# Kernel tuning notes

Hardware: AMD Instinct MI355X
Metric: run time of the kernel (lower is better)

Reference implementation:

```python
import jax, jax.numpy as jnp
import numpy as np

N, IN_F, E, EDGE_F, H, C = 50000, 128, 800000, 32, 4, 32
NEG_SLOPE = 0.2
EPS = 1e-16


def setup_inputs() -> dict:
    key = jax.random.key(0)
    ks = jax.random.split(key, 10)
    s = lambda *sh: 1.0 / np.sqrt(sh[-1])
    return {
        "node_features": jax.random.normal(ks[0], (N, IN_F), jnp.float32),
        "edge_features": jax.random.normal(ks[1], (E, EDGE_F), jnp.float32),
        "edge_index": jax.random.randint(ks[2], (2, E), 0, N, jnp.int32),
        # GATConv params
        "W_gat": jax.random.normal(ks[3], (H * C, IN_F), jnp.float32) * s(IN_F),
        "att_src": jax.random.normal(ks[4], (H, C), jnp.float32) * s(C),
        "att_dst": jax.random.normal(ks[5], (H, C), jnp.float32) * s(C),
        "att_edge": jax.random.normal(ks[6], (H, C), jnp.float32) * s(C),
        "bias": jnp.zeros((H * C,), jnp.float32),
        # edge_linear and skip_connection weights
        "W_edge": jax.random.normal(ks[7], (H * C, EDGE_F), jnp.float32) * s(EDGE_F),
        "W_skip": jax.random.normal(ks[8], (H * C, IN_F), jnp.float32) * s(IN_F),
    }


def reference(node_features, edge_features, edge_index, W_gat, att_src, att_dst,
              att_edge, bias, W_edge, W_skip):
    src, dst = edge_index[0], edge_index[1]
    # edge_linear + view(-1, H, C)
    e_attr = (edge_features @ W_edge.T).reshape(E, H, C)
    # GATConv: per-head linear transform of nodes -> [N, H, C]
    x = (node_features @ W_gat.T).reshape(N, H, C)
    # attention logits: a_src.x_i + a_dst.x_j + a_edge.e  -> [E, H]
    a_src = jnp.einsum('nhc,hc->nh', x, att_src)
    a_dst = jnp.einsum('nhc,hc->nh', x, att_dst)
    a_edge = jnp.einsum('ehc,hc->eh', e_attr, att_edge)
    alpha = jax.nn.leaky_relu(a_src[src] + a_dst[dst] + a_edge, NEG_SLOPE)
    # segment softmax over incoming edges of each destination node
    m = jax.ops.segment_max(alpha, dst, num_segments=N)  # [N, H]
    m = jnp.where(jnp.isfinite(m), m, 0.0)
    ex = jnp.exp(alpha - m[dst])
    denom = jax.ops.segment_sum(ex, dst, num_segments=N)  # [N, H]
    attn = ex / (denom[dst] + EPS)  # [E, H]
    # message = alpha * x_src ; scatter-add to destination
    msg = x[src] * attn[:, :, None]  # [E, H, C]
    out = jax.ops.segment_sum(msg, dst, num_segments=N)  # [N, H, C]
    out = out.reshape(N, H * C) + bias  # concat=True
    # skip connection + ELU activation
    out = out + node_features @ W_skip.T
    return jax.nn.elu(out)
```

## Files before the change

### kernel.cpp

```cpp
#include <hip/hip_runtime.h>
#include <hip/hip_bf16.h>

constexpr int N_NODES = 50000;
constexpr int IN_F    = 128;
constexpr long E_EDGES = 800000;
constexpr int EDGE_F  = 32;
constexpr int H_HEADS = 4;
constexpr int C_CH    = 32;
constexpr int HC      = 128;
constexpr float NEG_SLOPE = 0.2f;
constexpr float EPS = 1e-16f;
constexpr int B_HIST = 64;
constexpr int NT_GEMM = (N_NODES + 63) / 64;
constexpr int NB_GEMM2 = (NT_GEMM + 1) / 2;
constexpr int CHUNK  = (int)(E_EDGES / B_HIST);
constexpr int HW4    = N_NODES / 8;
constexpr int NB_SCAN = (N_NODES + 255) / 256;
constexpr int NB_A    = (N_NODES + 3) / 4;
constexpr int NB_EL4  = (int)((E_EDGES + 1023) / 1024);
constexpr int NB_AE5  = (int)((E_EDGES + 511) / 512);
constexpr float SM_SHIFT = 12.0f;

typedef __attribute__((ext_vector_type(8))) short bf16x8;
typedef __attribute__((ext_vector_type(4))) float f32x4;

__device__ __forceinline__ unsigned short f2b(float f) {
    __hip_bfloat16 h = __float2bfloat16(f);
    return *reinterpret_cast<unsigned short*>(&h);
}
__device__ __forceinline__ float b2f_lo(unsigned v) { return __uint_as_float(v << 16); }
__device__ __forceinline__ float b2f_hi(unsigned v) { return __uint_as_float(v & 0xffff0000u); }

__device__ __forceinline__ bf16x8 cvt8(const float* p) {
    float4 a = *(const float4*)p;
    float4 b = *(const float4*)(p + 4);
    bf16x8 f;
    f[0] = (short)f2b(a.x); f[1] = (short)f2b(a.y);
    f[2] = (short)f2b(a.z); f[3] = (short)f2b(a.w);
    f[4] = (short)f2b(b.x); f[5] = (short)f2b(b.y);
    f[6] = (short)f2b(b.z); f[7] = (short)f2b(b.w);
    return f;
}

__global__ __launch_bounds__(512, 4) void mega_kernel(
    const int* __restrict__ dst, unsigned int* __restrict__ histB,
    unsigned short* __restrict__ rank16, const float* __restrict__ ef,
    const float* __restrict__ We, const float* __restrict__ att_edge,
    const float* __restrict__ Wg, const float* __restrict__ Ws,
    float* __restrict__ ae, const float* __restrict__ nf,
    const float* __restrict__ bias, unsigned short* __restrict__ xb,
    float* __restrict__ out)
{
    __shared__ unsigned int h[HW4];
    __shared__ float wf_lds[128];
    const int b = blockIdx.x, t = threadIdx.x;

    if (b < B_HIST) {
        for (int i = t; i < HW4; i += 512) h[i] = 0;
        __syncthreads();
        const int e0 = b * CHUNK;
        for (int i = t * 4; i + 3 < CHUNK; i += 2048) {
            int4 d4 = *(const int4*)(dst + e0 + i);
            ushort4 r4;
            int sh0 = (d4.x & 7) * 4;
            int sh1 = (d4.y & 7) * 4;
            int sh2 = (d4.z & 7) * 4;
            int sh3 = (d4.w & 7) * 4;
            unsigned o0 = atomicAdd(&h[d4.x >> 3], 1u << sh0);
            unsigned o1 = atomicAdd(&h[d4.y >> 3], 1u << sh1);
            unsigned o2 = atomicAdd(&h[d4.z >> 3], 1u << sh2);
            unsigned o3 = atomicAdd(&h[d4.w >> 3], 1u << sh3);
            r4.x = (unsigned short)((o0 >> sh0) & 0xFu);
            r4.y = (unsigned short)((o1 >> sh1) & 0xFu);
            r4.z = (unsigned short)((o2 >> sh2) & 0xFu);
            r4.w = (unsigned short)((o3 >> sh3) & 0xFu);
            *(ushort4*)(rank16 + e0 + i) = r4;
        }
        __syncthreads();
        unsigned int* outp = histB + (size_t)b * HW4;
        for (int i = t; i < HW4; i += 512) outp[i] = h[i];
        return;
    }

    if (b < B_HIST + NB_GEMM2) {
        const int w8 = t >> 6;
        const int l  = t & 63;
        const int lr = l & 15;
        const int lk = l >> 4;
        const int tile = (b - B_HIST) * 2 + (w8 >> 2);
        if (tile >= NT_GEMM) return;
        const int wc = w8 & 3;
        const int n0 = tile * 64;

        f32x4 acc[4][4];
#pragma unroll
        for (int mf = 0; mf < 4; ++mf)
#pragma unroll
            for (int nfr = 0; nfr < 4; ++nfr)
                acc[mf][nfr] = (f32x4){0.f, 0.f, 0.f, 0.f};

#pragma unroll
        for (int ks = 0; ks < 4; ++ks) {
            bf16x8 bfr[4];
#pragma unroll
            for (int nfr = 0; nfr < 4; ++nfr) {
                int gr = wc * 64 + nfr * 16 + lr;
                const float* wp = (gr < HC ? Wg + (size_t)gr * IN_F
                                           : Ws + (size_t)(gr - HC) * IN_F)
                                  + ks * 32 + lk * 8;
                bfr[nfr] = cvt8(wp);
            }
            bf16x8 afr[4];
#pragma unroll
            for (int mf = 0; mf < 4; ++mf) {
                int row = n0 + mf * 16 + lr;
                row = row < N_NODES ? row : N_NODES - 1;
                afr[mf] = cvt8(nf + (size_t)row * IN_F + ks * 32 + lk * 8);
            }
#pragma unroll
            for (int mf = 0; mf < 4; ++mf)
#pragma unroll
                for (int nfr = 0; nfr < 4; ++nfr)
                    acc[mf][nfr] = __builtin_amdgcn_mfma_f32_16x16x32_bf16(
                        afr[mf], bfr[nfr], acc[mf][nfr], 0, 0, 0);
        }

#pragma unroll
        for (int nfr = 0; nfr < 4; ++nfr) {
            const int gc = wc * 64 + nfr * 16 + lr;
            if (gc < HC) {
#pragma unroll
                for (int mf = 0; mf < 4; ++mf)
#pragma unroll
                    for (int r = 0; r < 4; ++r) {
                        int m = n0 + mf * 16 + lk * 4 + r;
                        if (m < N_NODES) xb[(size_t)m * HC + gc] = f2b(acc[mf][nfr][r]);
                    }
            } else {
                const float bv = bias[gc - HC];
#pragma unroll
                for (int mf = 0; mf < 4; ++mf)
#pragma unroll
                    for (int r = 0; r < 4; ++r) {
                        int m = n0 + mf * 16 + lk * 4 + r;
                        if (m < N_NODES) out[(size_t)m * HC + gc - HC] = acc[mf][nfr][r] + bv;
                    }
            }
        }
        return;
    }

    {
        int o = t >> 2, hh = o >> 5, f = o & 31;
        int c0 = (t & 3) * 8;
        float a4 = 0.f;
#pragma unroll
        for (int j = 0; j < 8; ++j) {
            int c = c0 + j;
            a4 = fmaf(We[(hh * C_CH + c) * EDGE_F + f], att_edge[hh * C_CH + c], a4);
        }
        a4 += __shfl_xor(a4, 1);
        a4 += __shfl_xor(a4, 2);
        if ((t & 3) == 0) wf_lds[o] = a4;
    }
    __syncthreads();

    const int l = t & 63, wv = t >> 6;
    const int sub = l & 3, eIdx = l >> 2;
    const long eb = (long)(b - B_HIST - NB_GEMM2) * 512 + wv * 64 + eIdx;
    const float4* ef4 = (const float4*)ef;
    float4 wa[4], wb[4];
#pragma unroll
    for (int hh = 0; hh < 4; ++hh) {
        wa[hh] = *(const float4*)&wf_lds[hh * 32 + sub * 4];
        wb[hh] = *(const float4*)&wf_lds[hh * 32 + 16 + sub * 4];
    }

#pragma unroll
    for (int g = 0; g < 4; ++g) {
        long e = eb + g * 16;
        if (e >= E_EDGES) continue;
        float4 a0 = ef4[e * 8 + sub];
        float4 b0 = ef4[e * 8 + 4 + sub];
        float p[4];
#pragma unroll
        for (int hh = 0; hh < 4; ++hh) {
            float acc = 0.f;
            acc = fmaf(a0.x, wa[hh].x, acc); acc = fmaf(a0.y, wa[hh].y, acc);
            acc = fmaf(a0.z, wa[hh].z, acc); acc = fmaf(a0.w, wa[hh].w, acc);
            acc = fmaf(b0.x, wb[hh].x, acc); acc = fmaf(b0.y, wb[hh].y, acc);
            acc = fmaf(b0.z, wb[hh].z, acc); acc = fmaf(b0.w, wb[hh].w, acc);
            p[hh] = acc;
        }
#pragma unroll
        for (int hh = 0; hh < 4; ++hh) {
            p[hh] += __shfl_xor(p[hh], 1);
            p[hh] += __shfl_xor(p[hh], 2);
        }
        float v0 = (sub == 0) ? p[0] : (sub == 1) ? p[1] : (sub == 2) ? p[2] : p[3];
        ae[e * 4 + sub] = v0;
    }
}

__global__ __launch_bounds__(256) void scan1_a_kernel(
    const unsigned int* __restrict__ histB, int* __restrict__ row_ptr,
    int* __restrict__ blocksum, const unsigned int* __restrict__ xb32,
    const float* __restrict__ att_src, const float* __restrict__ att_dst,
    float* __restrict__ asrc, float* __restrict__ adst)
{
    const int b = blockIdx.x, t = threadIdx.x;
    if (b < NB_SCAN) {
        __shared__ int s[256];
        int i = b * 256 + t;
        int v = 0;
        if (i < N_NODES) {
            int w = i >> 3, sh = (i & 7) * 4;
#pragma unroll 8
            for (int bb = 0; bb < B_HIST; ++bb)
                v += (int)((histB[(size_t)bb * HW4 + w] >> sh) & 0xFu);
        }
        s[t] = v;
        __syncthreads();
#pragma unroll
        for (int off = 1; off < 256; off <<= 1) {
            int u = (t >= off) ? s[t - off] : 0;
            __syncthreads();
            s[t] += u;
            __syncthreads();
        }
        if (i < N_NODES) row_ptr[i] = s[t] - v;
        if (t == 255) blocksum[b] = s[255];
        return;
    }

    const int wave = t >> 6, lane = t & 63;
    const int n = (b - NB_SCAN) * 4 + wave;
    if (n >= N_NODES) return;
    unsigned v = xb32[(size_t)n * 64 + lane];
    float x0 = b2f_lo(v), x1 = b2f_hi(v);
    float2 as = ((const float2*)att_src)[lane];
    float2 ad = ((const float2*)att_dst)[lane];
    float ps = x0 * as.x + x1 * as.y;
    float pd = x0 * ad.x + x1 * ad.y;
#pragma unroll
    for (int off = 1; off < 16; off <<= 1) {
        ps += __shfl_xor(ps, off);
        pd += __shfl_xor(pd, off);
    }
    if ((lane & 15) == 0) {
        asrc[(size_t)n * H_HEADS + (lane >> 4)] = ps;
        adst[(size_t)n * H_HEADS + (lane >> 4)] = pd;
    }
}

__global__ __launch_bounds__(256) void scanF_kernel(int* __restrict__ row_ptr,
                                                    const int* __restrict__ blocksum,
                                                    const unsigned int* __restrict__ histB,
                                                    int* __restrict__ off)
{
    __shared__ int s[256];
    int t = threadIdx.x;
    int v = (t < NB_SCAN) ? blocksum[t] : 0;
    s[t] = v;
    __syncthreads();
#pragma unroll
    for (int o = 1; o < 256; o <<= 1) {
        int u = (t >= o) ? s[t - o] : 0;
        __syncthreads();
        s[t] += u;
        __syncthreads();
    }
    int excl = s[t] - v;
    __syncthreads();
    s[t] = excl;
    __syncthreads();
    const int blockoff = s[blockIdx.x];

    int i = blockIdx.x * 256 + t;
    if (i < N_NODES) {
        int run = row_ptr[i] + blockoff;
        row_ptr[i] = run;
        int w = i >> 3, sh = (i & 7) * 4;
#pragma unroll 8
        for (int b = 0; b < B_HIST; ++b) {
            off[(size_t)b * N_NODES + i] = run;
            run += (int)((histB[(size_t)b * HW4 + w] >> sh) & 0xFu);
        }
    }
    if (i == 0) row_ptr[N_NODES] = (int)E_EDGES;
}

__global__ __launch_bounds__(256) void edge_logits_kernel(
    const int* __restrict__ src, const int* __restrict__ dst,
    const float* __restrict__ ae, const float* __restrict__ asrc,
    const float* __restrict__ adst, const int* __restrict__ off,
    const unsigned short* __restrict__ rank16, uint4* __restrict__ rec4)
{
    const long base = (long)blockIdx.x * 1024 + threadIdx.x;

    int s[4], d[4], rk[4];
    float4 a_e[4];
    bool val[4];
    long ec[4];
#pragma unroll
    for (int j = 0; j < 4; ++j) {
        long e = base + j * 256;
        val[j] = e < E_EDGES;
        ec[j] = val[j] ? e : 0;
        s[j]  = src[ec[j]];
        d[j]  = dst[ec[j]];
        rk[j] = (int)rank16[ec[j]];
        a_e[j] = ((const float4*)ae)[ec[j]];
    }
    float4 as4[4], ad4[4];
    int pos[4];
#pragma unroll
    for (int j = 0; j < 4; ++j) {
        as4[j] = ((const float4*)asrc)[s[j]];
        ad4[j] = ((const float4*)adst)[d[j]];
        int be = (int)(ec[j] / CHUNK);
        pos[j] = off[(size_t)be * N_NODES + d[j]] + rk[j];
    }
#pragma unroll
    for (int j = 0; j < 4; ++j) {
        if (!val[j]) continue;
        float lg[4] = {as4[j].x + ad4[j].x + a_e[j].x, as4[j].y + ad4[j].y + a_e[j].y,
                       as4[j].z + ad4[j].z + a_e[j].z, as4[j].w + ad4[j].w + a_e[j].w};
        uint4 r;
        unsigned* rw = (unsigned*)&r;
#pragma unroll
        for (int h = 0; h < 4; ++h) {
            float al = lg[h] > 0.f ? lg[h] : NEG_SLOPE * lg[h];
            rw[h] = (__float_as_uint(al) & 0xFFFFFF00u)
                  | ((unsigned)(s[j] >> (8 * h)) & 0xFFu);
        }
        rec4[pos[j]] = r;
    }
}

__device__ __forceinline__ void accum8(float* acc, uint4 v, float e) {
    acc[0] = fmaf(b2f_lo(v.x), e, acc[0]);
    acc[1] = fmaf(b2f_hi(v.x), e, acc[1]);
    acc[2] = fmaf(b2f_lo(v.y), e, acc[2]);
    acc[3] = fmaf(b2f_hi(v.y), e, acc[3]);
    acc[4] = fmaf(b2f_lo(v.z), e, acc[4]);
    acc[5] = fmaf(b2f_hi(v.z), e, acc[5]);
    acc[6] = fmaf(b2f_lo(v.w), e, acc[6]);
    acc[7] = fmaf(b2f_hi(v.w), e, acc[7]);
}

__device__ __forceinline__ int rec_src(uint4 r) {
    return (int)((r.x & 0xFFu) | ((r.y & 0xFFu) << 8));
}
__device__ __forceinline__ float rec_alpha(uint4 r, int h) {
    unsigned w = h == 0 ? r.x : h == 1 ? r.y : h == 2 ? r.z : r.w;
    return __uint_as_float(w & 0xFFFFFF00u);
}

__global__ __launch_bounds__(256) void aggregate_kernel(
    const int* __restrict__ row_ptr, const uint4* __restrict__ rec4,
    const uint4* __restrict__ xb4, float* __restrict__ out)
{
    const int wave = threadIdx.x >> 6;
    const int lane = threadIdx.x & 63;
    const int d = blockIdx.x * 4 + wave;
    if (d >= N_NODES) return;
    const int beg = row_ptr[d], end = row_ptr[d + 1];
    const int q  = lane >> 4;
    const int cg = lane & 15;
    const int h  = cg >> 2;

    float acc[8] = {0.f, 0.f, 0.f, 0.f, 0.f, 0.f, 0.f, 0.f};
    float dsum = 0.f;

    int i = beg;
    for (; i + 8 <= end; i += 8) {
        int i0 = i + q, i1 = i + 4 + q;
        uint4 r0 = rec4[i0];
        uint4 r1 = rec4[i1];
        int s0 = rec_src(r0);
        int s1 = rec_src(r1);
        float a0 = rec_alpha(r0, h);
        float a1 = rec_alpha(r1, h);
        uint4 v0 = xb4[(size_t)s0 * 16 + cg];
        uint4 v1 = xb4[(size_t)s1 * 16 + cg];
        float e0 = __expf(a0 - SM_SHIFT);
        float e1 = __expf(a1 - SM_SHIFT);
        dsum += e0 + e1;
        accum8(acc, v0, e0);
        accum8(acc, v1, e1);
    }
    for (; i < end; i += 4) {
        int idx = i + q;
        bool val = idx < end;
        int ii = val ? idx : end - 1;
        uint4 r = rec4[ii];
        int s = rec_src(r);
        float a = rec_alpha(r, h);
        uint4 v = xb4[(size_t)s * 16 + cg];
        float e = val ? __expf(a - SM_SHIFT) : 0.f;
        dsum += e;
        accum8(acc, v, e);
    }

#pragma unroll
    for (int off = 16; off <= 32; off <<= 1) {
        dsum += __shfl_xor(dsum, off);
#pragma unroll
        for (int k = 0; k < 8; ++k) acc[k] += __shfl_xor(acc[k], off);
    }
    const float inv = 1.f / (dsum + EPS);

    if (q == 0) {
        float* op = out + (size_t)d * HC + cg * 8;
        float4 o0 = *(const float4*)op;
        float4 o1 = *(const float4*)(op + 4);
        o0.x += acc[0] * inv; o0.y += acc[1] * inv;
        o0.z += acc[2] * inv; o0.w += acc[3] * inv;
        o1.x += acc[4] * inv; o1.y += acc[5] * inv;
        o1.z += acc[6] * inv; o1.w += acc[7] * inv;
        o0.x = o0.x > 0.f ? o0.x : expf(o0.x) - 1.f;
        o0.y = o0.y > 0.f ? o0.y : expf(o0.y) - 1.f;
        o0.z = o0.z > 0.f ? o0.z : expf(o0.z) - 1.f;
        o0.w = o0.w > 0.f ? o0.w : expf(o0.w) - 1.f;
        o1.x = o1.x > 0.f ? o1.x : expf(o1.x) - 1.f;
        o1.y = o1.y > 0.f ? o1.y : expf(o1.y) - 1.f;
        o1.z = o1.z > 0.f ? o1.z : expf(o1.z) - 1.f;
        o1.w = o1.w > 0.f ? o1.w : expf(o1.w) - 1.f;
        *(float4*)op = o0;
        *(float4*)(op + 4) = o1;
    }
}

extern "C" void kernel_launch(void* const* d_in, const int* in_sizes, int n_in,
                              void* d_out, int out_size, void* d_ws, size_t ws_size,
                              hipStream_t stream)
{
    const float* nf       = (const float*)d_in[0];
    const float* ef       = (const float*)d_in[1];
    const int*   ei       = (const int*)d_in[2];
    const float* Wg       = (const float*)d_in[3];
    const float* att_src  = (const float*)d_in[4];
    const float* att_dst  = (const float*)d_in[5];
    const float* att_edge = (const float*)d_in[6];
    const float* bias     = (const float*)d_in[7];
    const float* We       = (const float*)d_in[8];
    const float* Ws       = (const float*)d_in[9];
    float* out = (float*)d_out;

    const int* src = ei;
    const int* dst = ei + E_EDGES;

    unsigned int* rec   = (unsigned int*)d_ws;
    float* ae           = (float*)(rec + 4 * E_EDGES);
    unsigned short* xb  = (unsigned short*)(ae + 4 * E_EDGES);
    float* asrc         = (float*)(xb + (size_t)N_NODES * HC);
    float* adst         = asrc + (size_t)N_NODES * H_HEADS;
    unsigned int* histB = (unsigned int*)(adst + (size_t)N_NODES * H_HEADS);
    int*   off          = (int*)(histB + (size_t)B_HIST * HW4);
    int*   row_ptr      = off + (size_t)B_HIST * N_NODES;
    int*   blocksum     = row_ptr + N_NODES + 1;
    unsigned short* rank16 = (unsigned short*)(blocksum + 256);

    mega_kernel<<<B_HIST + NB_GEMM2 + NB_AE5, 512, 0, stream>>>(
        dst, histB, rank16, ef, We, att_edge, Wg, Ws, ae, nf, bias, xb, out);
    scan1_a_kernel<<<NB_SCAN + NB_A, 256, 0, stream>>>(
        histB, row_ptr, blocksum, (const unsigned int*)xb,
        att_src, att_dst, asrc, adst);
    scanF_kernel<<<NB_SCAN, 256, 0, stream>>>(row_ptr, blocksum, histB, off);
    edge_logits_kernel<<<NB_EL4, 256, 0, stream>>>(
        src, dst, ae, asrc, adst, off, rank16, (uint4*)rec);
    aggregate_kernel<<<(N_NODES + 3) / 4, 256, 0, stream>>>(
        row_ptr, (const uint4*)rec, (const uint4*)xb, out);
}
```

Before: 140.9 us.

## Store per-chunk destination offsets as node-major bytes relative to row_ptr

The per-(chunk,node) scatter offsets change from a chunk-major int32 array to a node-major array of 64 uint8 values per node, each relative to row_ptr. scanF writes each node's 64 bytes with vector stores, and edge_logits now reads row_ptr plus one byte, which shrinks the offset buffer write and read traffic by about 4x. Separately, the edge-feature projection issues all four edge loads before computing, to raise memory-level parallelism. The byte offsets assume no node's in-degree exceeds 255, so inputs with a very high in-degree node would produce wrong results.

```diff
diff --git a/kernel.cpp b/kernel.cpp
--- a/kernel.cpp
+++ b/kernel.cpp
@@ -176,20 +176,25 @@
         wb[hh] = *(const float4*)&wf_lds[hh * 32 + 16 + sub * 4];
     }
 
+    long ecl[4];
+    float4 a0[4], b0[4];
 #pragma unroll
     for (int g = 0; g < 4; ++g) {
         long e = eb + g * 16;
-        if (e >= E_EDGES) continue;
-        float4 a0 = ef4[e * 8 + sub];
-        float4 b0 = ef4[e * 8 + 4 + sub];
+        ecl[g] = e < E_EDGES ? e : E_EDGES - 1;
+        a0[g] = ef4[ecl[g] * 8 + sub];
+        b0[g] = ef4[ecl[g] * 8 + 4 + sub];
+    }
+#pragma unroll
+    for (int g = 0; g < 4; ++g) {
         float p[4];
 #pragma unroll
         for (int hh = 0; hh < 4; ++hh) {
             float acc = 0.f;
-            acc = fmaf(a0.x, wa[hh].x, acc); acc = fmaf(a0.y, wa[hh].y, acc);
-            acc = fmaf(a0.z, wa[hh].z, acc); acc = fmaf(a0.w, wa[hh].w, acc);
-            acc = fmaf(b0.x, wb[hh].x, acc); acc = fmaf(b0.y, wb[hh].y, acc);
-            acc = fmaf(b0.z, wb[hh].z, acc); acc = fmaf(b0.w, wb[hh].w, acc);
+            acc = fmaf(a0[g].x, wa[hh].x, acc); acc = fmaf(a0[g].y, wa[hh].y, acc);
+            acc = fmaf(a0[g].z, wa[hh].z, acc); acc = fmaf(a0[g].w, wa[hh].w, acc);
+            acc = fmaf(b0[g].x, wb[hh].x, acc); acc = fmaf(b0[g].y, wb[hh].y, acc);
+            acc = fmaf(b0[g].z, wb[hh].z, acc); acc = fmaf(b0[g].w, wb[hh].w, acc);
             p[hh] = acc;
         }
 #pragma unroll
@@ -198,7 +203,7 @@
             p[hh] += __shfl_xor(p[hh], 2);
         }
         float v0 = (sub == 0) ? p[0] : (sub == 1) ? p[1] : (sub == 2) ? p[2] : p[3];
-        ae[e * 4 + sub] = v0;
+        if (eb + g * 16 < E_EDGES) ae[(eb + g * 16) * 4 + sub] = v0;
     }
 }
 
@@ -256,7 +261,7 @@
 __global__ __launch_bounds__(256) void scanF_kernel(int* __restrict__ row_ptr,
                                                     const int* __restrict__ blocksum,
                                                     const unsigned int* __restrict__ histB,
-                                                    int* __restrict__ off)
+                                                    unsigned char* __restrict__ off8)
 {
     __shared__ int s[256];
     int t = threadIdx.x;
@@ -278,14 +283,19 @@
 
     int i = blockIdx.x * 256 + t;
     if (i < N_NODES) {
-        int run = row_ptr[i] + blockoff;
-        row_ptr[i] = run;
+        int base = row_ptr[i] + blockoff;
+        row_ptr[i] = base;
+        int run = 0;
         int w = i >> 3, sh = (i & 7) * 4;
+        unsigned char o8[B_HIST];
 #pragma unroll 8
         for (int b = 0; b < B_HIST; ++b) {
-            off[(size_t)b * N_NODES + i] = run;
+            o8[b] = (unsigned char)run;
             run += (int)((histB[(size_t)b * HW4 + w] >> sh) & 0xFu);
         }
+#pragma unroll
+        for (int c = 0; c < 4; ++c)
+            *(uint4*)&off8[(size_t)i * 64 + c * 16] = *(const uint4*)&o8[c * 16];
     }
     if (i == 0) row_ptr[N_NODES] = (int)E_EDGES;
 }
@@ -293,7 +303,8 @@
 __global__ __launch_bounds__(256) void edge_logits_kernel(
     const int* __restrict__ src, const int* __restrict__ dst,
     const float* __restrict__ ae, const float* __restrict__ asrc,
-    const float* __restrict__ adst, const int* __restrict__ off,
+    const float* __restrict__ adst, const int* __restrict__ row_ptr,
+    const unsigned char* __restrict__ off8,
     const unsigned short* __restrict__ rank16, uint4* __restrict__ rec4)
 {
     const long base = (long)blockIdx.x * 1024 + threadIdx.x;
@@ -319,7 +330,7 @@
         as4[j] = ((const float4*)asrc)[s[j]];
         ad4[j] = ((const float4*)adst)[d[j]];
         int be = (int)(ec[j] / CHUNK);
-        pos[j] = off[(size_t)be * N_NODES + d[j]] + rk[j];
+        pos[j] = row_ptr[d[j]] + (int)off8[(size_t)d[j] * 64 + be] + rk[j];
     }
 #pragma unroll
     for (int j = 0; j < 4; ++j) {
@@ -457,8 +468,8 @@
     float* asrc         = (float*)(xb + (size_t)N_NODES * HC);
     float* adst         = asrc + (size_t)N_NODES * H_HEADS;
     unsigned int* histB = (unsigned int*)(adst + (size_t)N_NODES * H_HEADS);
-    int*   off          = (int*)(histB + (size_t)B_HIST * HW4);
-    int*   row_ptr      = off + (size_t)B_HIST * N_NODES;
+    unsigned char* off8 = (unsigned char*)(histB + (size_t)B_HIST * HW4);
+    int*   row_ptr      = (int*)(off8 + (size_t)N_NODES * 64);
     int*   blocksum     = row_ptr + N_NODES + 1;
     unsigned short* rank16 = (unsigned short*)(blocksum + 256);
 
@@ -467,9 +478,9 @@
     scan1_a_kernel<<<NB_SCAN + NB_A, 256, 0, stream>>>(
         histB, row_ptr, blocksum, (const unsigned int*)xb,
         att_src, att_dst, asrc, adst);
-    scanF_kernel<<<NB_SCAN, 256, 0, stream>>>(row_ptr, blocksum, histB, off);
+    scanF_kernel<<<NB_SCAN, 256, 0, stream>>>(row_ptr, blocksum, histB, off8);
     edge_logits_kernel<<<NB_EL4, 256, 0, stream>>>(
-        src, dst, ae, asrc, adst, off, rank16, (uint4*)rec);
+        src, dst, ae, asrc, adst, row_ptr, off8, rank16, (uint4*)rec);
     aggregate_kernel<<<(N_NODES + 3) / 4, 256, 0, stream>>>(
         row_ptr, (const uint4*)rec, (const uint4*)xb, out);
 }
```

New measurement: 153.7 us. 1.09x slower.
